# Kernel tuning notes

Measured on AMD Instinct MI355X. Metric: run time of the kernel, lower is better.

Reference implementation:

```python
import jax, jax.numpy as jnp
import numpy as np

T, D, E = 8192, 1024, 64
CAPACITY_FACTOR = 2.0
CAP = int(CAPACITY_FACTOR * np.ceil(T / E))  # 256 (training-mode capacity)
EPS = 1e-4


def setup_inputs() -> dict:
    key = jax.random.key(0)
    k1, k2, k3 = jax.random.split(key, 3)
    x = jax.random.normal(k1, (T, D), dtype=jnp.float32)
    W_red = jax.random.normal(k2, (D, 4), dtype=jnp.float32) * 0.02
    centroids = jax.random.normal(k3, (E, 4), dtype=jnp.float32)
    return {"x": x, "W_red": W_red, "centroids": centroids}


def reference(x, W_red, centroids):
    # dim reduction (nn.Linear(model_dim, 4, bias=False))
    red = x @ W_red  # [T, 4]
    # cosine logits: centroids are L2-normalized inside _cosine (the in-place
    # 1.5/norm rescale of the parameter cancels under F.normalize)
    c = centroids.astype(jnp.float32)
    cn = c / jnp.maximum(jnp.linalg.norm(c, axis=1, keepdims=True), EPS)
    logits = red.astype(jnp.float32) @ cn.T  # [T, E]
    # _make_finite
    finite = jnp.isfinite(logits)
    fmin = jnp.min(jnp.where(finite, logits, jnp.inf))
    logits = jnp.where(finite, logits, fmin)

    gates = jax.nn.softmax(logits, axis=1)                 # [T, E]
    idx1 = jnp.argmax(gates, axis=1)                       # [T]
    mask1 = jax.nn.one_hot(idx1, E, dtype=gates.dtype)     # [T, E]
    expert_counts = jnp.sum(mask1, axis=0).astype(jnp.int32)  # metadata

    gates1_s = 1.5 * jnp.sum(gates * mask1, axis=1)        # [T]
    loc1 = jnp.cumsum(mask1, axis=0) - 1.0                 # positions within expert

    me = jnp.mean(gates, axis=0)
    ce = jnp.mean(mask1, axis=0)
    l_aux = jnp.mean(me * ce) * (E * E)

    mask1 = mask1 * (loc1 < CAP).astype(mask1.dtype)       # drop overflow tokens
    loc1_s = jnp.sum(loc1 * mask1, axis=1).astype(jnp.int32)  # [T]
    gates1 = gates1_s[:, None] * mask1                     # [T, E]
    loc_sc = jax.nn.one_hot(loc1_s, CAP, dtype=gates1.dtype)  # [T, CAP]
    combine = gates1[:, :, None] * loc_sc[:, None, :]      # [T, E, CAP]
    dispatch_mask = combine != 0
    return (l_aux, combine.astype(x.dtype), dispatch_mask, expert_counts)
```

## Files before the change

### kernel.cpp

```cpp
#include <hip/hip_runtime.h>

#define T 8192
#define D 1024
#define E 64
#define CAP 256

typedef float f32x4 __attribute__((ext_vector_type(4)));

static const size_t TEC = (size_t)T * E * CAP;
#define C_OFF   ((size_t)1)
#define M_OFF   ((size_t)1 + (size_t)T * E * CAP)
#define CNT_OFF ((size_t)1 + 2 * (size_t)T * E * CAP)

__global__ __launch_bounds__(256) void k1_gate(
    const float* __restrict__ x, const float* __restrict__ Wred,
    const float* __restrict__ cent, int* __restrict__ idx1,
    float* __restrict__ g15, float* __restrict__ Sg, int* __restrict__ bc)
{
    __shared__ float wcol[4 * D];
    __shared__ float cn[E * 4];
    __shared__ float sg[E];
    const int tid = threadIdx.x;

    for (int i = tid; i < 4 * D; i += 256) {
        int d = i >> 2, c = i & 3;
        wcol[c * D + d] = Wred[i];
    }
    if (tid < E) {
        float c0 = cent[tid * 4 + 0];
        float c1 = cent[tid * 4 + 1];
        float c2 = cent[tid * 4 + 2];
        float c3 = cent[tid * 4 + 3];
        float n = fmaxf(sqrtf(c0 * c0 + c1 * c1 + c2 * c2 + c3 * c3), 1e-4f);
        cn[tid * 4 + 0] = c0 / n;
        cn[tid * 4 + 1] = c1 / n;
        cn[tid * 4 + 2] = c2 / n;
        cn[tid * 4 + 3] = c3 / n;
        sg[tid] = 0.0f;
    }
    __syncthreads();

    const int wave = tid >> 6, lane = tid & 63;
    for (int it = 0; it < 4; ++it) {
        const int t = blockIdx.x * 16 + it * 4 + wave;
        const float* xr = x + (size_t)t * D;
        float a0 = 0.f, a1 = 0.f, a2 = 0.f, a3 = 0.f;
        #pragma unroll
        for (int k = 0; k < 16; ++k) {
            int d = k * 64 + lane;
            float xv = xr[d];
            a0 += xv * wcol[d];
            a1 += xv * wcol[D + d];
            a2 += xv * wcol[2 * D + d];
            a3 += xv * wcol[3 * D + d];
        }
        #pragma unroll
        for (int off = 32; off; off >>= 1) {
            a0 += __shfl_xor(a0, off);
            a1 += __shfl_xor(a1, off);
            a2 += __shfl_xor(a2, off);
            a3 += __shfl_xor(a3, off);
        }
        float logit = a0 * cn[lane * 4 + 0] + a1 * cn[lane * 4 + 1]
                    + a2 * cn[lane * 4 + 2] + a3 * cn[lane * 4 + 3];
        float m = logit;
        #pragma unroll
        for (int off = 32; off; off >>= 1) m = fmaxf(m, __shfl_xor(m, off));
        unsigned long long ball = __ballot(logit == m);
        int amax = __ffsll(ball) - 1;
        float ev = expf(logit - m);
        float s = ev;
        #pragma unroll
        for (int off = 32; off; off >>= 1) s += __shfl_xor(s, off);
        atomicAdd(&sg[lane], ev / s);
        if (lane == 0) {
            idx1[t] = amax;
            g15[t] = 1.5f / s;
            atomicAdd(&bc[(t >> 8) * E + amax], 1);
        }
    }
    __syncthreads();
    if (tid < E) atomicAdd(&Sg[tid], sg[tid]);
}

__global__ __launch_bounds__(64) void k3_prefix(const int* __restrict__ bc,
                                                int* __restrict__ pf,
                                                const float* __restrict__ Sg,
                                                float* __restrict__ out)
{
    const int e = threadIdx.x;
    int run = 0;
    for (int b = 0; b < 32; ++b) {
        pf[b * E + e] = run;
        run += bc[b * E + e];
    }
    out[CNT_OFF + e] = (float)run;
    float v = Sg[e] * (float)run;
    #pragma unroll
    for (int off = 32; off; off >>= 1) v += __shfl_xor(v, off);
    if (e == 0) out[0] = v * ((float)E / ((float)T * (float)T));
}

__global__ __launch_bounds__(256) void k4_fill_scatter(
    const int* __restrict__ idx1, const float* __restrict__ g15,
    const int* __restrict__ pf, float* __restrict__ out)
{
    const int tid = threadIdx.x;
    const int t = blockIdx.x;
    const int chunk = t >> 8;
    const int tin = t & 255;

    __shared__ int ids[256];
    __shared__ int wsum[4];
    const int e = idx1[t];
    ids[tid] = idx1[chunk * 256 + tid];
    __syncthreads();
    int flag = (tid < tin && ids[tid] == e) ? 1 : 0;
    unsigned long long b = __ballot(flag != 0);
    if ((tid & 63) == 0) wsum[tid >> 6] = __popcll(b);
    __syncthreads();
    const int rank = pf[chunk * E + e] + wsum[0] + wsum[1] + wsum[2] + wsum[3];

    float* __restrict__ crow = out + C_OFF + (size_t)t * (E * CAP);
    float* __restrict__ mrow = out + M_OFF + (size_t)t * (E * CAP);
    const f32x4 z4 = {0.f, 0.f, 0.f, 0.f};
    #pragma unroll
    for (int k = 0; k < 16; ++k) {
        int i = tid + k * 256;
        if (i < 4095) {
            __builtin_nontemporal_store(z4, (f32x4*)(crow + 3 + 4 * (size_t)i));
            __builtin_nontemporal_store(z4, (f32x4*)(mrow + 3 + 4 * (size_t)i));
        }
    }
    if (tid == 0) {
        crow[0] = 0.f; crow[1] = 0.f; crow[2] = 0.f; crow[16383] = 0.f;
        mrow[0] = 0.f; mrow[1] = 0.f; mrow[2] = 0.f; mrow[16383] = 0.f;
    }
    __syncthreads();
    if (tid == 0 && rank < CAP) {
        size_t o = (size_t)e * CAP + rank;
        crow[o] = g15[t];
        mrow[o] = 1.0f;
    }
}

extern "C" void kernel_launch(void* const* d_in, const int* in_sizes, int n_in,
                              void* d_out, int out_size, void* d_ws, size_t ws_size,
                              hipStream_t stream)
{
    const float* x    = (const float*)d_in[0];
    const float* Wred = (const float*)d_in[1];
    const float* cent = (const float*)d_in[2];
    float* out = (float*)d_out;

    char* ws = (char*)d_ws;
    int*   idx1 = (int*)ws;
    float* g15  = (float*)(ws + 32768);
    float* Sg   = (float*)(ws + 65536);
    int*   bc   = (int*)(ws + 65536 + 256);
    int*   pf   = (int*)(ws + 65536 + 256 + 8192);

    (void)hipMemsetAsync(Sg, 0, 256 + 32 * E * sizeof(int), stream);

    k1_gate<<<512, 256, 0, stream>>>(x, Wred, cent, idx1, g15, Sg, bc);
    k3_prefix<<<1, 64, 0, stream>>>(bc, pf, Sg, out);
    k4_fill_scatter<<<T, 256, 0, stream>>>(idx1, g15, pf, out);
}
```

Baseline: 1.163 ms.

## Fuse output zero-fill into gate kernel and merge prefix with scatter

The gate kernel now runs one token per wave across 2048 blocks. After gating, each block zero-fills a contiguous 512KB slice of the whole combine/dispatch output using coalesced vector stores. The old per-token fill kernel, which re-read the chunk's indices for every token, is removed. A new 32-block kernel computes per-chunk prefix offsets and within-wave ranks using ballots, then scatters the single nonzero per token and writes counts and l_aux. This cuts a launch and the redundant rank work, but drops nontemporal stores and makes the fill a flat memset whose bandwidth depends on the store pattern.

```diff
diff --git a/kernel.cpp b/kernel.cpp
--- a/kernel.cpp
+++ b/kernel.cpp
@@ -7,15 +7,16 @@
 
 typedef float f32x4 __attribute__((ext_vector_type(4)));
 
-static const size_t TEC = (size_t)T * E * CAP;
+#define TEC ((size_t)134217728)
 #define C_OFF   ((size_t)1)
-#define M_OFF   ((size_t)1 + (size_t)T * E * CAP)
-#define CNT_OFF ((size_t)1 + 2 * (size_t)T * E * CAP)
+#define M_OFF   ((size_t)1 + TEC)
+#define CNT_OFF ((size_t)1 + 2 * TEC)
 
-__global__ __launch_bounds__(256) void k1_gate(
+__global__ __launch_bounds__(256) void kA_gate_fill(
     const float* __restrict__ x, const float* __restrict__ Wred,
     const float* __restrict__ cent, int* __restrict__ idx1,
-    float* __restrict__ g15, float* __restrict__ Sg, int* __restrict__ bc)
+    float* __restrict__ g15, float* __restrict__ Sg, int* __restrict__ bc,
+    float* __restrict__ out)
 {
     __shared__ float wcol[4 * D];
     __shared__ float cn[E * 4];
@@ -41,8 +42,8 @@
     __syncthreads();
 
     const int wave = tid >> 6, lane = tid & 63;
-    for (int it = 0; it < 4; ++it) {
-        const int t = blockIdx.x * 16 + it * 4 + wave;
+    const int t = blockIdx.x * 4 + wave;
+    {
         const float* xr = x + (size_t)t * D;
         float a0 = 0.f, a1 = 0.f, a2 = 0.f, a3 = 0.f;
         #pragma unroll
@@ -81,66 +82,71 @@
     }
     __syncthreads();
     if (tid < E) atomicAdd(&Sg[tid], sg[tid]);
+
+    const f32x4 z4 = {0.f, 0.f, 0.f, 0.f};
+    f32x4* __restrict__ base = (f32x4*)(out + 4);
+    const size_t b0 = (size_t)blockIdx.x * 32768;
+    #pragma unroll 4
+    for (int k = 0; k < 128; ++k) {
+        size_t fi = b0 + (size_t)k * 256 + tid;
+        if (fi < (size_t)67108863) base[fi] = z4;
+    }
+    if (blockIdx.x == 0 && tid < 4) {
+        if (tid < 3) out[1 + tid] = 0.f;
+        else         out[2 * TEC] = 0.f;
+    }
 }
 
-__global__ __launch_bounds__(64) void k3_prefix(const int* __restrict__ bc,
-                                                int* __restrict__ pf,
-                                                const float* __restrict__ Sg,
-                                                float* __restrict__ out)
+__global__ __launch_bounds__(256) void k5_prefix_patch(
+    const int* __restrict__ idx1, const float* __restrict__ g15,
+    const int* __restrict__ bc, const float* __restrict__ Sg,
+    float* __restrict__ out)
 {
-    const int e = threadIdx.x;
-    int run = 0;
-    for (int b = 0; b < 32; ++b) {
-        pf[b * E + e] = run;
-        run += bc[b * E + e];
+    __shared__ int pfe[E];
+    __shared__ int cwf[256];
+    const int tid = threadIdx.x;
+    const int chunk = blockIdx.x;
+    const int t = chunk * 256 + tid;
+    const int e = idx1[t];
+
+    if (tid < E) {
+        int run = 0;
+        for (int b = 0; b < chunk; ++b) run += bc[b * E + tid];
+        pfe[tid] = run;
     }
-    out[CNT_OFF + e] = (float)run;
-    float v = Sg[e] * (float)run;
+    cwf[tid] = 0;
+    __syncthreads();
+
+    const int wave = tid >> 6, lane = tid & 63;
+    unsigned long long same = ~0ull;
     #pragma unroll
-    for (int off = 32; off; off >>= 1) v += __shfl_xor(v, off);
-    if (e == 0) out[0] = v * ((float)E / ((float)T * (float)T));
-}
+    for (int b = 0; b < 6; ++b) {
+        unsigned long long bal = __ballot(((e >> b) & 1) != 0);
+        same &= ((e >> b) & 1) ? bal : ~bal;
+    }
+    const unsigned long long below = ((unsigned long long)1 << lane) - 1ull;
+    const int rank_in_wave = __popcll(same & below);
+    if ((same & below) == 0ull) cwf[wave * E + e] = __popcll(same);
+    __syncthreads();
 
-__global__ __launch_bounds__(256) void k4_fill_scatter(
-    const int* __restrict__ idx1, const float* __restrict__ g15,
-    const int* __restrict__ pf, float* __restrict__ out)
-{
-    const int tid = threadIdx.x;
-    const int t = blockIdx.x;
-    const int chunk = t >> 8;
-    const int tin = t & 255;
+    int rank = pfe[e] + rank_in_wave;
+    if (wave > 0) rank += cwf[0 * E + e];
+    if (wave > 1) rank += cwf[1 * E + e];
+    if (wave > 2) rank += cwf[2 * E + e];
 
-    __shared__ int ids[256];
-    __shared__ int wsum[4];
-    const int e = idx1[t];
-    ids[tid] = idx1[chunk * 256 + tid];
-    __syncthreads();
-    int flag = (tid < tin && ids[tid] == e) ? 1 : 0;
-    unsigned long long b = __ballot(flag != 0);
-    if ((tid & 63) == 0) wsum[tid >> 6] = __popcll(b);
-    __syncthreads();
-    const int rank = pf[chunk * E + e] + wsum[0] + wsum[1] + wsum[2] + wsum[3];
+    if (rank < CAP) {
+        const size_t row = (size_t)t * (E * CAP) + (size_t)e * CAP + rank;
+        out[C_OFF + row] = g15[t];
+        out[M_OFF + row] = 1.0f;
+    }
 
-    float* __restrict__ crow = out + C_OFF + (size_t)t * (E * CAP);
-    float* __restrict__ mrow = out + M_OFF + (size_t)t * (E * CAP);
-    const f32x4 z4 = {0.f, 0.f, 0.f, 0.f};
-    #pragma unroll
-    for (int k = 0; k < 16; ++k) {
-        int i = tid + k * 256;
-        if (i < 4095) {
-            __builtin_nontemporal_store(z4, (f32x4*)(crow + 3 + 4 * (size_t)i));
-            __builtin_nontemporal_store(z4, (f32x4*)(mrow + 3 + 4 * (size_t)i));
-        }
-    }
-    if (tid == 0) {
-        crow[0] = 0.f; crow[1] = 0.f; crow[2] = 0.f; crow[16383] = 0.f;
-        mrow[0] = 0.f; mrow[1] = 0.f; mrow[2] = 0.f; mrow[16383] = 0.f;
-    }
-    __syncthreads();
-    if (tid == 0 && rank < CAP) {
-        size_t o = (size_t)e * CAP + rank;
-        crow[o] = g15[t];
-        mrow[o] = 1.0f;
+    if (chunk == 31 && tid < E) {
+        int total = pfe[tid] + bc[31 * E + tid];
+        out[CNT_OFF + tid] = (float)total;
+        float v = Sg[tid] * (float)total;
+        #pragma unroll
+        for (int off = 32; off; off >>= 1) v += __shfl_xor(v, off);
+        if (tid == 0) out[0] = v * ((float)E / ((float)T * (float)T));
     }
 }
 
@@ -158,11 +164,9 @@
     float* g15  = (float*)(ws + 32768);
     float* Sg   = (float*)(ws + 65536);
     int*   bc   = (int*)(ws + 65536 + 256);
-    int*   pf   = (int*)(ws + 65536 + 256 + 8192);
 
     (void)hipMemsetAsync(Sg, 0, 256 + 32 * E * sizeof(int), stream);
 
-    k1_gate<<<512, 256, 0, stream>>>(x, Wred, cent, idx1, g15, Sg, bc);
-    k3_prefix<<<1, 64, 0, stream>>>(bc, pf, Sg, out);
-    k4_fill_scatter<<<T, 256, 0, stream>>>(idx1, g15, pf, out);
+    kA_gate_fill<<<2048, 256, 0, stream>>>(x, Wred, cent, idx1, g15, Sg, bc, out);
+    k5_prefix_patch<<<32, 256, 0, stream>>>(idx1, g15, bc, Sg, out);
 }
```

Result: faster. 1.093 ms (-6.1%).
